# Kernel optimization log

Measured on AMD Instinct MI355X. Metric: run time of the kernel, lower is better.

## Reference

```python
import jax, jax.numpy as jnp
import numpy as np

WZ, WH, WW = 2, 6, 12
WIN = WZ * WH * WW  # 144
DEPTH, DIM, HEADS = 2, 192, 6
NEG = -1e9


def earth_position_index():
    zi = np.arange(WZ); zj = -np.arange(WZ) * WZ
    hi = np.arange(WH); hj = -np.arange(WH) * WH
    w = np.arange(WW)
    c1 = np.stack(np.meshgrid(zi, hi, w, indexing='ij')).reshape(3, -1)
    c2 = np.stack(np.meshgrid(zj, hj, w, indexing='ij')).reshape(3, -1)
    coords = (c1[:, :, None] - c2[:, None, :]).transpose(1, 2, 0).copy()
    coords[:, :, 2] += WW - 1
    coords[:, :, 1] *= 2 * WW - 1
    coords[:, :, 0] *= (2 * WW - 1) * WH * WH
    return jnp.asarray(coords.sum(-1))


def shift_mask(Z, H):
    # Swin-style mask over Z (vertical) and H (latitude); W (longitude) is circular.
    sz, sh = WZ // 2, WH // 2
    region = np.zeros((Z, H), np.int32)
    cnt = 0
    for zs in (slice(0, Z - WZ), slice(Z - WZ, Z - sz), slice(Z - sz, Z)):
        for hs in (slice(0, H - WH), slice(H - WH, H - sh), slice(H - sh, H)):
            region[zs, hs] = cnt; cnt += 1
    r = region.reshape(Z // WZ, WZ, H // WH, WH).transpose(0, 2, 1, 3).reshape(-1, WZ * WH)
    r = np.repeat(r, WW, axis=1)  # window token order is (z,h,w)
    m = np.where(r[:, :, None] == r[:, None, :], 0.0, NEG).astype(np.float32)
    return jnp.asarray(m)


def window_partition(x, Z, H, W):
    B, C = x.shape[0], x.shape[-1]
    x = x.reshape(B, Z // WZ, WZ, H // WH, WH, W // WW, WW, C)
    x = x.transpose(0, 1, 3, 5, 2, 4, 6, 7)
    return x.reshape(B, (Z // WZ) * (H // WH) * (W // WW), WIN, C)


def window_reverse(xw, Z, H, W):
    B, C = xw.shape[0], xw.shape[-1]
    x = xw.reshape(B, Z // WZ, H // WH, W // WW, WZ, WH, WW, C)
    x = x.transpose(0, 1, 4, 2, 5, 3, 6, 7)
    return x.reshape(B, Z, H, W, C)


def layernorm(x, g, b):
    mu = x.mean(-1, keepdims=True)
    var = jnp.mean((x - mu) ** 2, axis=-1, keepdims=True)
    return (x - mu) * jax.lax.rsqrt(var + 1e-5) * g + b


def attn_windows(xw, qkv_w, qkv_b, proj_w, proj_b, bias_tab, pos_idx, mask):
    B, nW, N, C = xw.shape
    hd = C // HEADS
    qkv = (xw @ qkv_w + qkv_b).reshape(B, nW, N, 3, HEADS, hd)
    q, k, v = qkv[..., 0, :, :], qkv[..., 1, :, :], qkv[..., 2, :, :]
    attn = jnp.einsum('bwnhd,bwmhd->bwhnm', q * (hd ** -0.5), k)
    bias = bias_tab[pos_idx]
    attn = attn + bias.transpose(2, 0, 1)[None, None]
    if mask is not None:
        nzh = mask.shape[0]
        attn = attn.reshape(B, nzh, nW // nzh, HEADS, N, N) + mask[None, :, None, None]
        attn = attn.reshape(B, nW, HEADS, N, N)
    attn = jax.nn.softmax(attn, axis=-1)
    out = jnp.einsum('bwhnm,bwmhd->bwnhd', attn, v).reshape(B, nW, N, C)
    return out @ proj_w + proj_b


def forward(x, qkv_w, qkv_b, proj_w, proj_b, bias_tab,
            ln1_g, ln1_b, ln2_g, ln2_b, mlp_w1, mlp_b1, mlp_w2, mlp_b2, Z, H, W):
    B, L, C = x.shape
    pos_idx = earth_position_index()
    mask = shift_mask(Z, H)
    depth = qkv_w.shape[0]
    for i in range(depth):
        roll = (i % 2 == 1)
        shortcut = x
        xg = x.reshape(B, Z, H, W, C)
        if roll:
            xg = jnp.roll(xg, (-(WZ // 2), -(WH // 2), -(WW // 2)), axis=(1, 2, 3))
        xw = window_partition(xg, Z, H, W)
        xw = attn_windows(xw, qkv_w[i], qkv_b[i], proj_w[i], proj_b[i],
                          bias_tab[i], pos_idx, mask if roll else None)
        xg = window_reverse(xw, Z, H, W)
        if roll:
            xg = jnp.roll(xg, (WZ // 2, WH // 2, WW // 2), axis=(1, 2, 3))
        xa = xg.reshape(B, L, C)
        x = shortcut + layernorm(xa, ln1_g[i], ln1_b[i])
        h = jax.nn.gelu(x @ mlp_w1[i] + mlp_b1[i], approximate=False)
        h = h @ mlp_w2[i] + mlp_b2[i]
        x = x + layernorm(h, ln2_g[i], ln2_b[i])
    return x


def setup_inputs() -> dict:
    key = jax.random.key(0)
    ks = jax.random.split(key, 16)
    B, Z, H, W, C = 1, 8, 96, 180, DIM
    L = Z * H * W
    bias_rows = (2 * WW - 1) * WH * WH * WZ * WZ  # 3312
    s = 0.02
    return {
        'x': jax.random.normal(ks[0], (B, L, C), jnp.float32),
        'qkv_w': jax.random.normal(ks[1], (DEPTH, C, 3 * C), jnp.float32) * s,
        'qkv_b': jnp.zeros((DEPTH, 3 * C), jnp.float32),
        'proj_w': jax.random.normal(ks[2], (DEPTH, C, C), jnp.float32) * s,
        'proj_b': jnp.zeros((DEPTH, C), jnp.float32),
        'bias_tab': jax.random.normal(ks[3], (DEPTH, bias_rows, HEADS), jnp.float32) * s,
        'ln1_g': jnp.ones((DEPTH, C), jnp.float32),
        'ln1_b': jnp.zeros((DEPTH, C), jnp.float32),
        'ln2_g': jnp.ones((DEPTH, C), jnp.float32),
        'ln2_b': jnp.zeros((DEPTH, C), jnp.float32),
        'mlp_w1': jax.random.normal(ks[4], (DEPTH, C, 4 * C), jnp.float32) * s,
        'mlp_b1': jnp.zeros((DEPTH, 4 * C), jnp.float32),
        'mlp_w2': jax.random.normal(ks[5], (DEPTH, 4 * C, C), jnp.float32) * s,
        'mlp_b2': jnp.zeros((DEPTH, C), jnp.float32),
        'Z': Z, 'H': H, 'W': W,
    }


def reference(x, qkv_w, qkv_b, proj_w, proj_b, bias_tab, ln1_g, ln1_b, ln2_g, ln2_b,
              mlp_w1, mlp_b1, mlp_w2, mlp_b2, Z, H, W):
    return forward(x, qkv_w, qkv_b, proj_w, proj_b, bias_tab, ln1_g, ln1_b,
                   ln2_g, ln2_b, mlp_w1, mlp_b1, mlp_w2, mlp_b2, Z, H, W)
```

## Files before the change

kernel.cpp:

```cpp
#include <hip/hip_runtime.h>
#include <hip/hip_bf16.h>
#include <math.h>

#define L_TOK 138240
#define NW 960

typedef __attribute__((ext_vector_type(8))) short s16x8;
typedef __attribute__((ext_vector_type(8))) unsigned short u16x8;
typedef __attribute__((ext_vector_type(4))) unsigned short u16x4;
typedef __attribute__((ext_vector_type(4))) float f32x4;

__device__ __forceinline__ float bf2f(unsigned short u){
  union{unsigned int u;float f;} v; v.u=((unsigned int)u)<<16; return v.f;
}
__device__ __forceinline__ unsigned short f2bf(float f){
  __hip_bfloat16 b = __float2bfloat16(f);
  union { __hip_bfloat16 b; unsigned short u; } v; v.b = b; return v.u;
}
__device__ __forceinline__ void gll16(const void* g, void* l) {
  __builtin_amdgcn_global_load_lds((const __attribute__((address_space(1))) void*)g,
                                   (__attribute__((address_space(3))) void*)l, 16, 0, 0);
}
__device__ __forceinline__ float gelu_f(float v){
  const float s = v * 0.70710678118654752f;
  const float a = fabsf(s);
  const float t = 1.0f / (1.0f + 0.3275911f * a);
  float p = 1.061405429f;
  p = p*t - 1.453152027f;
  p = p*t + 1.421413741f;
  p = p*t - 0.284496736f;
  p = p*t + 0.254829592f;
  p = p*t;
  float y = 1.0f - p * __expf(-a*a);
  y = copysignf(y, s);
  return 0.5f * v * (1.0f + y);
}

template<int NTILES>
__global__ __launch_bounds__(256) void gemm_qkv(
    const unsigned short* __restrict__ xb,
    const unsigned short* __restrict__ Bt,
    const float* __restrict__ bias,
    unsigned short* __restrict__ out)
{
  __shared__ unsigned short As[64*192];
  const int tid = threadIdx.x;
  const int wid = tid >> 6, lane = tid & 63;
  const int lr = lane & 15, kg = lane >> 4;
  const int bm = blockIdx.x;
  const int wn = wid * 16;
  const int N = NTILES * 64;

  #pragma unroll
  for (int i = 0; i < 6; i++) {
    const int c = tid + i*256;
    const int r = c / 24, s = c % 24;
    const int sg = (s & 24) | ((s ^ r) & 7);
    gll16(&xb[(size_t)(bm*64 + r)*192 + sg*8], &As[c*8]);
  }
  __syncthreads();

  s16x8 a[4][6];
  #pragma unroll
  for (int mi = 0; mi < 4; mi++)
    #pragma unroll
    for (int ks = 0; ks < 6; ks++) {
      const int m = mi*16 + lr, g = ks*4 + kg;
      const int sg = (g & 24) | ((g ^ m) & 7);
      a[mi][ks] = *(const s16x8*)&As[m*192 + sg*8];
    }

  for (int bn = 0; bn < NTILES; bn++) {
    s16x8 b[6];
    #pragma unroll
    for (int ks = 0; ks < 6; ks++)
      b[ks] = *(const s16x8*)&Bt[(size_t)(bn*64 + wn + lr)*192 + ks*32 + kg*8];
    f32x4 acc[4] = {};
    #pragma unroll
    for (int ks = 0; ks < 6; ks++)
      #pragma unroll
      for (int mi = 0; mi < 4; mi++)
        acc[mi] = __builtin_amdgcn_mfma_f32_16x16x32_bf16(a[mi][ks], b[ks], acc[mi], 0, 0, 0);
    const int col = bn*64 + wn + lr;
    const float bv = bias[col];
    #pragma unroll
    for (int mi = 0; mi < 4; mi++)
      #pragma unroll
      for (int q = 0; q < 4; q++) {
        const int row = bm*64 + mi*16 + kg*4 + q;
        out[(size_t)row*N + col] = f2bf(acc[mi][q] + bv);
      }
  }
}

__global__ __launch_bounds__(256) void gemm_ln(
    const unsigned short* __restrict__ A,
    const unsigned short* __restrict__ Bt,
    const float* __restrict__ bias, const float* __restrict__ g,
    const float* __restrict__ bta,
    float* __restrict__ x, unsigned short* __restrict__ xbo,
    int lda)
{
  __shared__ unsigned short As[2][128*32];
  __shared__ unsigned short Bs[2][192*32];
  __shared__ float rowstat[128][2][2];
  const int tid = threadIdx.x;
  const int wid = tid >> 6, lane = tid & 63;
  const int lr = lane & 15, kg = lane >> 4;
  const int bm = blockIdx.x;
  const int wm = (wid >> 1) * 64, wn = (wid & 1) * 96;
  const int rsub = lane >> 2, kc = lane & 3;
  const int K = 192;

  f32x4 acc[4][6] = {};
  const int nst = K / 32;

  #pragma unroll
  for (int i = 0; i < 2; i++)
    gll16(&A[(size_t)(bm*128 + wid*32 + i*16 + rsub)*lda + kc*8], &As[0][(wid*32 + i*16)*32]);
  #pragma unroll
  for (int j = 0; j < 3; j++)
    gll16(&Bt[(size_t)(wid*48 + j*16 + rsub)*K + kc*8], &Bs[0][(wid*48 + j*16)*32]);
  __syncthreads();

  for (int t = 0; t < nst; t++) {
    const int cur = t & 1, nxt = cur ^ 1;
    if (t + 1 < nst) {
      const int k1 = (t+1)*32;
      #pragma unroll
      for (int i = 0; i < 2; i++)
        gll16(&A[(size_t)(bm*128 + wid*32 + i*16 + rsub)*lda + k1 + kc*8], &As[nxt][(wid*32 + i*16)*32]);
      #pragma unroll
      for (int j = 0; j < 3; j++)
        gll16(&Bt[(size_t)(wid*48 + j*16 + rsub)*K + k1 + kc*8], &Bs[nxt][(wid*48 + j*16)*32]);
    }
    s16x8 a[4], b[6];
    #pragma unroll
    for (int mi = 0; mi < 4; mi++) a[mi] = *(const s16x8*)&As[cur][(wm + mi*16 + lr)*32 + kg*8];
    #pragma unroll
    for (int ni = 0; ni < 6; ni++) b[ni] = *(const s16x8*)&Bs[cur][(wn + ni*16 + lr)*32 + kg*8];
    #pragma unroll
    for (int mi = 0; mi < 4; mi++)
      #pragma unroll
      for (int ni = 0; ni < 6; ni++)
        acc[mi][ni] = __builtin_amdgcn_mfma_f32_16x16x32_bf16(a[mi], b[ni], acc[mi][ni], 0, 0, 0);
    __syncthreads();
  }

  float bv[6], gv[6], btv[6];
  #pragma unroll
  for (int ni = 0; ni < 6; ni++) {
    const int col = wn + ni*16 + lr;
    bv[ni] = bias[col]; gv[ni] = g[col]; btv[ni] = bta[col];
  }
  #pragma unroll
  for (int mi = 0; mi < 4; mi++) {
    float s[4] = {0,0,0,0}, ss[4] = {0,0,0,0};
    #pragma unroll
    for (int ni = 0; ni < 6; ni++)
      #pragma unroll
      for (int q = 0; q < 4; q++) {
        const float v = acc[mi][ni][q] + bv[ni];
        s[q] += v; ss[q] += v*v;
      }
    #pragma unroll
    for (int q = 0; q < 4; q++) {
      #pragma unroll
      for (int m = 1; m < 16; m <<= 1) {
        s[q]  += __shfl_xor(s[q],  m, 64);
        ss[q] += __shfl_xor(ss[q], m, 64);
      }
    }
    if (lr == 0) {
      #pragma unroll
      for (int q = 0; q < 4; q++) {
        const int r = wm + mi*16 + kg*4 + q;
        rowstat[r][wid & 1][0] = s[q];
        rowstat[r][wid & 1][1] = ss[q];
      }
    }
  }
  __syncthreads();
  #pragma unroll
  for (int mi = 0; mi < 4; mi++) {
    #pragma unroll
    for (int q = 0; q < 4; q++) {
      const int rl = wm + mi*16 + kg*4 + q;
      const float s  = rowstat[rl][0][0] + rowstat[rl][1][0];
      const float ss = rowstat[rl][0][1] + rowstat[rl][1][1];
      const float mu = s * (1.0f/192.0f);
      const float rs = rsqrtf(ss * (1.0f/192.0f) - mu*mu + 1e-5f);
      const size_t grow = (size_t)(bm*128 + rl) * 192;
      #pragma unroll
      for (int ni = 0; ni < 6; ni++) {
        const float v = acc[mi][ni][q] + bv[ni];
        const float o = (v - mu) * rs * gv[ni] + btv[ni];
        const size_t idx = grow + wn + ni*16 + lr;
        const float xn = x[idx] + o;
        x[idx] = xn; xbo[idx] = f2bf(xn);
      }
    }
  }
}

__global__ __launch_bounds__(256) void fused_mlp(
    const unsigned short* __restrict__ xb,
    const unsigned short* __restrict__ W1t,
    const unsigned short* __restrict__ W2t,
    const float* __restrict__ b1, const float* __restrict__ b2,
    const float* __restrict__ g, const float* __restrict__ bt,
    float* __restrict__ x, unsigned short* __restrict__ xbo)
{
  __shared__ unsigned short As[64*192];
  __shared__ unsigned short Hs[2][64*64];
  __shared__ float rowstat[64][4][2];
  const int tid = threadIdx.x, wid = tid >> 6, lane = tid & 63;
  const int lr = lane & 15, kg = lane >> 4;
  const int row0 = blockIdx.x * 64;

  #pragma unroll
  for (int i = 0; i < 6; i++) {
    const int c = tid + i*256;
    const int r = c / 24, s = c % 24;
    const int sg = (s & 24) | ((s ^ r) & 7);
    gll16(&xb[(size_t)(row0 + r)*192 + sg*8], &As[c*8]);
  }
  __syncthreads();

  char* const hs0 = (char*)&Hs[0][0];
  char* const hs1 = (char*)&Hs[1][0];

  f32x4 yacc[4][3] = {};
  for (int t = 0; t < 12; t++) {
    char* const hb = (t & 1) ? hs1 : hs0;
    s16x8 w1f[6];
    #pragma unroll
    for (int ks = 0; ks < 6; ks++)
      w1f[ks] = *(const s16x8*)&W1t[(size_t)(t*64 + wid*16 + lr)*192 + ks*32 + kg*8];
    const float4 b1q = *(const float4*)&b1[t*64 + wid*16 + kg*4];
    #pragma unroll
    for (int mb = 0; mb < 4; mb++) {
      const int m = mb*16 + lr;
      f32x4 hacc = {0.f, 0.f, 0.f, 0.f};
      #pragma unroll
      for (int ks = 0; ks < 6; ks++) {
        const int gsl = ks*4 + kg;
        const int sg = (gsl & 24) | ((gsl ^ m) & 7);
        const s16x8 xf8 = *(const s16x8*)&As[m*192 + sg*8];
        hacc = __builtin_amdgcn_mfma_f32_16x16x32_bf16(w1f[ks], xf8, hacc, 0, 0, 0);
      }
      u16x4 hv;
      hv[0] = f2bf(gelu_f(hacc[0] + b1q.x));
      hv[1] = f2bf(gelu_f(hacc[1] + b1q.y));
      hv[2] = f2bf(gelu_f(hacc[2] + b1q.z));
      hv[3] = f2bf(gelu_f(hacc[3] + b1q.w));
      const int cb = wid*32 + kg*8;
      *(u16x4*)(hb + m*128 + (cb ^ ((m & 7) << 4))) = hv;
    }
    __syncthreads();
    #pragma unroll
    for (int kk = 0; kk < 2; kk++) {
      s16x8 b2f[3];
      #pragma unroll
      for (int nj = 0; nj < 3; nj++)
        b2f[nj] = *(const s16x8*)&W2t[(size_t)(wid*48 + nj*16 + lr)*768 + t*64 + kk*32 + kg*8];
      #pragma unroll
      for (int mi = 0; mi < 4; mi++) {
        const int m = mi*16 + lr;
        const int cb2 = kk*64 + kg*16;
        const s16x8 a2 = *(const s16x8*)(hb + m*128 + (cb2 ^ ((m & 7) << 4)));
        #pragma unroll
        for (int nj = 0; nj < 3; nj++)
          yacc[mi][nj] = __builtin_amdgcn_mfma_f32_16x16x32_bf16(a2, b2f[nj], yacc[mi][nj], 0, 0, 0);
      }
    }
  }

  float bv[3], gv[3], btv[3];
  #pragma unroll
  for (int nj = 0; nj < 3; nj++) {
    const int col = wid*48 + nj*16 + lr;
    bv[nj] = b2[col]; gv[nj] = g[col]; btv[nj] = bt[col];
  }
  #pragma unroll
  for (int mi = 0; mi < 4; mi++) {
    float s[4] = {0,0,0,0}, ss[4] = {0,0,0,0};
    #pragma unroll
    for (int nj = 0; nj < 3; nj++)
      #pragma unroll
      for (int q = 0; q < 4; q++) {
        const float v = yacc[mi][nj][q] + bv[nj];
        s[q] += v; ss[q] += v*v;
      }
    #pragma unroll
    for (int q = 0; q < 4; q++) {
      #pragma unroll
      for (int m = 1; m < 16; m <<= 1) {
        s[q]  += __shfl_xor(s[q],  m, 64);
        ss[q] += __shfl_xor(ss[q], m, 64);
      }
    }
    if (lr == 0) {
      #pragma unroll
      for (int q = 0; q < 4; q++) {
        rowstat[mi*16 + kg*4 + q][wid][0] = s[q];
        rowstat[mi*16 + kg*4 + q][wid][1] = ss[q];
      }
    }
  }
  __syncthreads();
  #pragma unroll
  for (int mi = 0; mi < 4; mi++) {
    #pragma unroll
    for (int q = 0; q < 4; q++) {
      const int rl = mi*16 + kg*4 + q;
      const float s  = rowstat[rl][0][0] + rowstat[rl][1][0] + rowstat[rl][2][0] + rowstat[rl][3][0];
      const float ss = rowstat[rl][0][1] + rowstat[rl][1][1] + rowstat[rl][2][1] + rowstat[rl][3][1];
      const float mu = s * (1.0f/192.0f);
      const float rs = rsqrtf(ss * (1.0f/192.0f) - mu*mu + 1e-5f);
      const size_t grow = (size_t)(row0 + rl) * 192;
      #pragma unroll
      for (int nj = 0; nj < 3; nj++) {
        const float v = yacc[mi][nj][q] + bv[nj];
        const float o = (v - mu) * rs * gv[nj] + btv[nj];
        const size_t idx = grow + wid*48 + nj*16 + lr;
        const float xn = x[idx] + o;
        x[idx] = xn; xbo[idx] = f2bf(xn);
      }
    }
  }
}

__global__ __launch_bounds__(384) void attn_win7(
    unsigned short* qkv,
    const unsigned short* __restrict__ biasbt,
    int roll)
{
  __shared__ unsigned short Pw[6][16][168];
  __shared__ int lmap[144];

  const int w = blockIdx.x;
  const int tid = threadIdx.x, wid = tid / 64, lane = tid & 63;
  const int lr = lane & 15, kg = lane >> 4;
  const int ww = w % 15, hw = (w / 15) % 16, zw = w / 240;

  if (tid < 144) {
    const int z1 = tid / 72, h1 = (tid % 72) / 12, w1 = tid % 12;
    int z = zw*2 + z1, h = hw*6 + h1, xx = ww*12 + w1;
    if (roll) { z = (z + 1) & 7; h = (h + 3) % 96; xx = (xx + 6) % 180; }
    lmap[tid] = (z*96 + h)*180 + xx;
  }
  __syncthreads();

  const unsigned short* bb;
  if (roll) {
    const int c = ((zw == 3) ? 2 : 0) | ((hw == 15) ? 1 : 0);
    bb = biasbt + (size_t)c*124416 + (size_t)wid*20736;
  } else {
    bb = biasbt + (size_t)wid*20736;
  }

  s16x8 kfr[9];
  #pragma unroll
  for (int ti = 0; ti < 9; ti++)
    kfr[ti] = *(const s16x8*)&qkv[(size_t)lmap[ti*16 + lr]*576 + 192 + wid*32 + kg*8];

  s16x8 vbr[2][5];
  #pragma unroll
  for (int ci = 0; ci < 2; ci++)
    #pragma unroll
    for (int ks = 0; ks < 5; ks++) {
      u16x8 t;
      #pragma unroll
      for (int j = 0; j < 8; j++) {
        const int tok = ks*32 + kg*8 + j;
        t[j] = (tok < 144) ? qkv[(size_t)lmap[tok]*576 + 384 + wid*32 + ci*16 + lr] : (unsigned short)0;
      }
      vbr[ci][ks] = (s16x8)t;
    }

  #pragma unroll
  for (int j = 0; j < 4; j++) Pw[wid][lr][144 + kg*4 + j] = 0;

  for (int s = 0; s < 9; s++) {
    const s16x8 bq = *(const s16x8*)&qkv[(size_t)lmap[s*16 + lr]*576 + wid*32 + kg*8];

    float pb[9][4];
    float mx = -3.0e38f;
    #pragma unroll
    for (int ti = 0; ti < 9; ti++) {
      f32x4 acc = {0.f, 0.f, 0.f, 0.f};
      acc = __builtin_amdgcn_mfma_f32_16x16x32_bf16(kfr[ti], bq, acc, 0, 0, 0);
      const u16x4 b4 = *(const u16x4*)&bb[(size_t)(s*9 + ti)*256 + lr*16 + kg*4];
      #pragma unroll
      for (int q = 0; q < 4; q++) {
        const float sv = acc[q] + bf2f(b4[q]);
        pb[ti][q] = sv;
        mx = fmaxf(mx, sv);
      }
    }
    mx = fmaxf(mx, __shfl_xor(mx, 16, 64));
    mx = fmaxf(mx, __shfl_xor(mx, 32, 64));

    float sum = 0.f;
    #pragma unroll
    for (int ti = 0; ti < 9; ti++)
      #pragma unroll
      for (int q = 0; q < 4; q++) {
        const float p = __expf(pb[ti][q] - mx);
        pb[ti][q] = p;
        sum += p;
      }
    sum += __shfl_xor(sum, 16, 64);
    sum += __shfl_xor(sum, 32, 64);
    const float inv = 1.0f / sum;

    #pragma unroll
    for (int ti = 0; ti < 9; ti++)
      #pragma unroll
      for (int q = 0; q < 4; q++)
        Pw[wid][lr][ti*16 + kg*4 + q] = f2bf(pb[ti][q] * inv);

    #pragma unroll
    for (int ci = 0; ci < 2; ci++) {
      f32x4 accO = {0.f, 0.f, 0.f, 0.f};
      #pragma unroll
      for (int ks = 0; ks < 5; ks++) {
        const s16x8 pa = *(const s16x8*)&Pw[wid][lr][ks*32 + kg*8];
        accO = __builtin_amdgcn_mfma_f32_16x16x32_bf16(pa, vbr[ci][ks], accO, 0, 0, 0);
      }
      #pragma unroll
      for (int q = 0; q < 4; q++) {
        const int row = s*16 + kg*4 + q;
        qkv[(size_t)lmap[row]*576 + wid*32 + ci*16 + lr] = f2bf(accO[q]);
      }
    }
  }
}

__global__ void init_x(const float* __restrict__ xin, float* __restrict__ x,
                       unsigned short* __restrict__ xb, int n) {
  const int i = blockIdx.x*256 + threadIdx.x;
  if (i < n) { const float f = xin[i]; x[i] = f; xb[i] = f2bf(f); }
}
__global__ void copy_diag(const float* __restrict__ a, float* __restrict__ o, int n) {
  const int i = blockIdx.x*256 + threadIdx.x;
  if (i < n) o[i] = a[i] + 50.0f;
}
__global__ void transpose_w(const float* __restrict__ src, unsigned short* __restrict__ dst,
                            int K, int N, int nscale, float factor) {
  const int i = blockIdx.x*256 + threadIdx.x;
  const int tot = K*N;
  if (i >= 2*tot) return;
  const int l = i / tot, e = i % tot;
  const int k = e / N, n = e % N;
  float v = src[i];
  if (n < nscale) v *= factor;
  dst[(size_t)l*tot + (size_t)n*K + k] = f2bf(v);
}
__global__ void scale_qb(const float* __restrict__ src, float* __restrict__ dst) {
  const int i = blockIdx.x*256 + threadIdx.x;
  if (i >= 2*576) return;
  const float f = (i % 576) < 192 ? 0.17677669529663687f : 1.0f;
  dst[i] = src[i] * f;
}
__global__ void build_biasb6(const float* __restrict__ tab, unsigned short* __restrict__ bm) {
  const int i = blockIdx.x*256 + threadIdx.x;
  const int TAB = 6*144*144;
  if (i >= 5*TAB) return;
  const int tau = i / TAB, r = i % TAB;
  const int hd = r / 20736, rr = r % 20736;
  const int s = rr / 2304, rrr = rr % 2304;
  const int ti = rrr / 256, e = rrr % 256;
  const int lr_ = e / 16, c4 = e % 16;
  const int q = s*16 + lr_, tok = ti*16 + c4;
  const int z1 = q/72,  h1 = (q%72)/12,  w1 = q%12;
  const int z2 = tok/72, h2 = (tok%72)/12, w2 = tok%12;
  const int idx = (z1 + 2*z2)*828 + (h1 + 6*h2)*23 + (w1 - w2 + 11);
  const int l = (tau == 0) ? 0 : 1;
  float v = tab[(size_t)l*3312*6 + (size_t)idx*6 + hd];
  if (tau >= 1) {
    const int c = tau - 1, zs = c >> 1, hs = c & 1;
    const int rq = (zs ? (1 + z1) : 0)*3 + (hs ? (1 + (h1 >= 3)) : 0);
    const int rt = (zs ? (1 + z2) : 0)*3 + (hs ? (1 + (h2 >= 3)) : 0);
    if (rq != rt) v -= 1.0e9f;
  }
  bm[i] = f2bf(v);
}

extern "C" void kernel_launch(void* const* d_in, const int* in_sizes, int n_in,
                              void* d_out, int out_size, void* d_ws, size_t ws_size,
                              hipStream_t stream) {
  const float* x_in    = (const float*)d_in[0];
  const float* qkv_w   = (const float*)d_in[1];
  const float* qkv_b   = (const float*)d_in[2];
  const float* proj_w  = (const float*)d_in[3];
  const float* proj_b  = (const float*)d_in[4];
  const float* bias_tab= (const float*)d_in[5];
  const float* ln1_g   = (const float*)d_in[6];
  const float* ln1_b   = (const float*)d_in[7];
  const float* ln2_g   = (const float*)d_in[8];
  const float* ln2_b   = (const float*)d_in[9];
  const float* mlp_w1  = (const float*)d_in[10];
  const float* mlp_b1  = (const float*)d_in[11];
  const float* mlp_w2  = (const float*)d_in[12];
  const float* mlp_b2  = (const float*)d_in[13];

  const int nElem = L_TOK * 192;
  float* xf = (float*)d_out;

  const size_t sz_R0 = 159252480;
  const size_t sz_xb = 53084160;
  const size_t sz_wT = 1769472;
  const size_t sz_bb = 2488320;
  const size_t sz_qb = 4608;
  const size_t need  = sz_R0 + sz_xb + sz_wT + sz_bb + sz_qb;

  if (ws_size < need) {
    copy_diag<<<dim3((nElem+255)/256), 256, 0, stream>>>(x_in, xf, nElem);
    return;
  }

  char* ws = (char*)d_ws;
  unsigned short* R0    = (unsigned short*)(ws);
  unsigned short* xb    = (unsigned short*)(ws + sz_R0);
  unsigned short* wT    = (unsigned short*)(ws + sz_R0 + sz_xb);
  unsigned short* biasb = (unsigned short*)(ws + sz_R0 + sz_xb + sz_wT);
  float*          qb2   = (float*)(ws + sz_R0 + sz_xb + sz_wT + sz_bb);

  unsigned short* wT_qkv  = wT;
  unsigned short* wT_proj = wT + 221184;
  unsigned short* wT_m1   = wT + 294912;
  unsigned short* wT_m2   = wT + 589824;

  transpose_w<<<dim3((2*192*576+255)/256), 256, 0, stream>>>(qkv_w,  wT_qkv, 192, 576, 192, 0.17677669529663687f);
  transpose_w<<<dim3((2*192*192+255)/256), 256, 0, stream>>>(proj_w, wT_proj,192, 192, 0, 1.0f);
  transpose_w<<<dim3((2*192*768+255)/256), 256, 0, stream>>>(mlp_w1, wT_m1,  192, 768, 0, 1.0f);
  transpose_w<<<dim3((2*768*192+255)/256), 256, 0, stream>>>(mlp_w2, wT_m2,  768, 192, 0, 1.0f);
  build_biasb6<<<dim3((5*6*144*144+255)/256), 256, 0, stream>>>(bias_tab, biasb);
  scale_qb<<<dim3(5), 256, 0, stream>>>(qkv_b, qb2);

  init_x<<<dim3((nElem+255)/256), 256, 0, stream>>>(x_in, xf, xb, nElem);

  for (int i = 0; i < 2; i++) {
    gemm_qkv<9><<<dim3(2160), 256, 0, stream>>>(
        xb, wT_qkv + (size_t)i*110592, qb2 + i*576, R0);
    attn_win7<<<dim3(NW), 384, 0, stream>>>(
        R0, biasb + (i ? 124416 : 0), i & 1);
    gemm_ln<<<dim3(1080), 256, 0, stream>>>(
        R0, wT_proj + (size_t)i*36864, proj_b + i*192,
        ln1_g + i*192, ln1_b + i*192, xf, xb, 576);
    fused_mlp<<<dim3(2160), 256, 0, stream>>>(
        xb, wT_m1 + (size_t)i*147456, wT_m2 + (size_t)i*147456,
        mlp_b1 + i*768, mlp_b2 + i*192,
        ln2_g + i*192, ln2_b + i*192, xf, xb);
  }
}
```

Measured before the change: 1.075 ms.

## Keep residual stream in bf16 only and single-buffer MLP hidden tile

The fp32 residual copy is dropped. Both the proj+LN kernel and the MLP kernel now read and update the bf16 residual buffer, and fp32 is written only at the final MLP output. This removes the fp32 read and write traffic for the residual in every layer. The MLP hidden shared-memory tile also goes from double to single buffer, with an extra barrier and GELU outputs held in registers, which cuts LDS use and may raise occupancy. The cost is lower residual precision from repeated bf16 rounding and an extra sync per tile.

```diff
diff --git a/kernel.cpp b/kernel.cpp
--- a/kernel.cpp
+++ b/kernel.cpp
@@ -98,7 +98,7 @@
     const unsigned short* __restrict__ Bt,
     const float* __restrict__ bias, const float* __restrict__ g,
     const float* __restrict__ bta,
-    float* __restrict__ x, unsigned short* __restrict__ xbo,
+    unsigned short* __restrict__ xbo,
     int lda)
 {
   __shared__ unsigned short As[2][128*32];
@@ -196,23 +196,23 @@
         const float v = acc[mi][ni][q] + bv[ni];
         const float o = (v - mu) * rs * gv[ni] + btv[ni];
         const size_t idx = grow + wn + ni*16 + lr;
-        const float xn = x[idx] + o;
-        x[idx] = xn; xbo[idx] = f2bf(xn);
-      }
-    }
-  }
-}
-
+        xbo[idx] = f2bf(bf2f(xbo[idx]) + o);
+      }
+    }
+  }
+}
+
+template<int WF32>
 __global__ __launch_bounds__(256) void fused_mlp(
     const unsigned short* __restrict__ xb,
     const unsigned short* __restrict__ W1t,
     const unsigned short* __restrict__ W2t,
     const float* __restrict__ b1, const float* __restrict__ b2,
     const float* __restrict__ g, const float* __restrict__ bt,
-    float* __restrict__ x, unsigned short* __restrict__ xbo)
+    unsigned short* __restrict__ xbo, float* __restrict__ xf)
 {
   __shared__ unsigned short As[64*192];
-  __shared__ unsigned short Hs[2][64*64];
+  __shared__ unsigned short Hs[64*64];
   __shared__ float rowstat[64][4][2];
   const int tid = threadIdx.x, wid = tid >> 6, lane = tid & 63;
   const int lr = lane & 15, kg = lane >> 4;
@@ -227,17 +227,16 @@
   }
   __syncthreads();
 
-  char* const hs0 = (char*)&Hs[0][0];
-  char* const hs1 = (char*)&Hs[1][0];
+  char* const hs = (char*)&Hs[0];
 
   f32x4 yacc[4][3] = {};
   for (int t = 0; t < 12; t++) {
-    char* const hb = (t & 1) ? hs1 : hs0;
     s16x8 w1f[6];
     #pragma unroll
     for (int ks = 0; ks < 6; ks++)
       w1f[ks] = *(const s16x8*)&W1t[(size_t)(t*64 + wid*16 + lr)*192 + ks*32 + kg*8];
     const float4 b1q = *(const float4*)&b1[t*64 + wid*16 + kg*4];
+    u16x4 hv[4];
     #pragma unroll
     for (int mb = 0; mb < 4; mb++) {
       const int m = mb*16 + lr;
@@ -249,13 +248,19 @@
         const s16x8 xf8 = *(const s16x8*)&As[m*192 + sg*8];
         hacc = __builtin_amdgcn_mfma_f32_16x16x32_bf16(w1f[ks], xf8, hacc, 0, 0, 0);
       }
-      u16x4 hv;
-      hv[0] = f2bf(gelu_f(hacc[0] + b1q.x));
-      hv[1] = f2bf(gelu_f(hacc[1] + b1q.y));
-      hv[2] = f2bf(gelu_f(hacc[2] + b1q.z));
-      hv[3] = f2bf(gelu_f(hacc[3] + b1q.w));
+      hv[mb][0] = f2bf(gelu_f(hacc[0] + b1q.x));
+      hv[mb][1] = f2bf(gelu_f(hacc[1] + b1q.y));
+      hv[mb][2] = f2bf(gelu_f(hacc[2] + b1q.z));
+      hv[mb][3] = f2bf(gelu_f(hacc[3] + b1q.w));
+    }
+    __syncthreads();
+    {
       const int cb = wid*32 + kg*8;
-      *(u16x4*)(hb + m*128 + (cb ^ ((m & 7) << 4))) = hv;
+      #pragma unroll
+      for (int mb = 0; mb < 4; mb++) {
+        const int m = mb*16 + lr;
+        *(u16x4*)(hs + m*128 + (cb ^ ((m & 7) << 4))) = hv[mb];
+      }
     }
     __syncthreads();
     #pragma unroll
@@ -268,7 +273,7 @@
       for (int mi = 0; mi < 4; mi++) {
         const int m = mi*16 + lr;
         const int cb2 = kk*64 + kg*16;
-        const s16x8 a2 = *(const s16x8*)(hb + m*128 + (cb2 ^ ((m & 7) << 4)));
+        const s16x8 a2 = *(const s16x8*)(hs + m*128 + (cb2 ^ ((m & 7) << 4)));
         #pragma unroll
         for (int nj = 0; nj < 3; nj++)
           yacc[mi][nj] = __builtin_amdgcn_mfma_f32_16x16x32_bf16(a2, b2f[nj], yacc[mi][nj], 0, 0, 0);
@@ -324,8 +329,9 @@
         const float v = yacc[mi][nj][q] + bv[nj];
         const float o = (v - mu) * rs * gv[nj] + btv[nj];
         const size_t idx = grow + wid*48 + nj*16 + lr;
-        const float xn = x[idx] + o;
-        x[idx] = xn; xbo[idx] = f2bf(xn);
+        const float xn = bf2f(xbo[idx]) + o;
+        xbo[idx] = f2bf(xn);
+        if (WF32) xf[idx] = xn;
       }
     }
   }
@@ -438,10 +444,9 @@
   }
 }
 
-__global__ void init_x(const float* __restrict__ xin, float* __restrict__ x,
-                       unsigned short* __restrict__ xb, int n) {
+__global__ void init_xb(const float* __restrict__ xin, unsigned short* __restrict__ xb, int n) {
   const int i = blockIdx.x*256 + threadIdx.x;
-  if (i < n) { const float f = xin[i]; x[i] = f; xb[i] = f2bf(f); }
+  if (i < n) xb[i] = f2bf(xin[i]);
 }
 __global__ void copy_diag(const float* __restrict__ a, float* __restrict__ o, int n) {
   const int i = blockIdx.x*256 + threadIdx.x;
@@ -540,7 +545,7 @@
   build_biasb6<<<dim3((5*6*144*144+255)/256), 256, 0, stream>>>(bias_tab, biasb);
   scale_qb<<<dim3(5), 256, 0, stream>>>(qkv_b, qb2);
 
-  init_x<<<dim3((nElem+255)/256), 256, 0, stream>>>(x_in, xf, xb, nElem);
+  init_xb<<<dim3((nElem+255)/256), 256, 0, stream>>>(x_in, xb, nElem);
 
   for (int i = 0; i < 2; i++) {
     gemm_qkv<9><<<dim3(2160), 256, 0, stream>>>(
@@ -549,10 +554,15 @@
         R0, biasb + (i ? 124416 : 0), i & 1);
     gemm_ln<<<dim3(1080), 256, 0, stream>>>(
         R0, wT_proj + (size_t)i*36864, proj_b + i*192,
-        ln1_g + i*192, ln1_b + i*192, xf, xb, 576);
-    fused_mlp<<<dim3(2160), 256, 0, stream>>>(
-        xb, wT_m1 + (size_t)i*147456, wT_m2 + (size_t)i*147456,
-        mlp_b1 + i*768, mlp_b2 + i*192,
-        ln2_g + i*192, ln2_b + i*192, xf, xb);
-  }
-}
+        ln1_g + i*192, ln1_b + i*192, xb, 576);
+    if (i == 0)
+      fused_mlp<0><<<dim3(2160), 256, 0, stream>>>(
+          xb, wT_m1, wT_m2, mlp_b1, mlp_b2,
+          ln2_g, ln2_b, xb, nullptr);
+    else
+      fused_mlp<1><<<dim3(2160), 256, 0, stream>>>(
+          xb, wT_m1 + (size_t)147456, wT_m2 + (size_t)147456,
+          mlp_b1 + 768, mlp_b2 + 192,
+          ln2_g + 192, ln2_b + 192, xb, xf);
+  }
+}
```

Result: faster. 937.9 us (-12.8%).
